# Kernel tuning notes

Hardware: AMD Instinct MI355X
Metric: run time of the kernel (lower is better)

Reference implementation:

```python
import jax, jax.numpy as jnp
import numpy as np
from jax.ops import segment_sum, segment_max

N_GENE, D_IN, HID, HEADS = 100000, 128, 128, 4
N_DRUG, N_DIS = 10000, 5000


def gcn_conv(x, src, dst, W, b, n):
    # PyG GCNConv: add self loops, symmetric deg^-1/2 normalization, scatter-add
    h = x @ W  # [n, hid]
    loop = jnp.arange(n)
    s = jnp.concatenate([src, loop])
    d = jnp.concatenate([dst, loop])
    deg = segment_sum(jnp.ones(d.shape[0], h.dtype), d, num_segments=n)
    dis = jnp.where(deg > 0, jax.lax.rsqrt(deg), 0.0)
    norm = dis[s] * dis[d]  # [E+n]
    return segment_sum(h[s] * norm[:, None], d, num_segments=n) + b


def gat_conv(xs, xd, src, dst, W, att_s, att_d, b, n_dst, heads=HEADS):
    # PyG GATConv (bipartite, shared lin, add_self_loops=False, concat=False)
    C = W.shape[1] // heads
    hs = (xs @ W).reshape(-1, heads, C)  # [Ns,H,C]
    hd = (xd @ W).reshape(-1, heads, C)  # [Nd,H,C]
    a_s = (hs * att_s).sum(-1)  # [Ns,H]
    a_d = (hd * att_d).sum(-1)  # [Nd,H]
    e = jax.nn.leaky_relu(a_s[src] + a_d[dst], 0.2)  # [E,H]
    m = segment_max(e, dst, num_segments=n_dst)
    m = jnp.where(jnp.isfinite(m), m, 0.0)
    ex = jnp.exp(e - m[dst])
    denom = segment_sum(ex, dst, num_segments=n_dst)
    alpha = ex / (denom[dst] + 1e-16)  # per-dst softmax
    out = segment_sum(hs[src] * alpha[:, :, None], dst, num_segments=n_dst)  # [Nd,H,C]
    return out.mean(axis=1) + b


def setup_inputs() -> dict:
    key = jax.random.key(0)
    ks = jax.random.split(key, 24)
    Eg, Ed, Ec = 1000000, 250000, 250000
    sc = 1.0 / np.sqrt(HID)
    inp = {
        'gene_nodes': jax.random.normal(ks[0], (N_GENE, D_IN), jnp.float32),
        'drug_edges': jnp.stack([jax.random.randint(ks[1], (Ed,), 0, N_DRUG),
                                 jax.random.randint(ks[2], (Ed,), 0, N_GENE)]),
        'disease_edges': jnp.stack([jax.random.randint(ks[3], (Ec,), 0, N_DIS),
                                    jax.random.randint(ks[4], (Ec,), 0, N_GENE)]),
        'gene_edges': jax.random.randint(ks[5], (2, Eg), 0, N_GENE),
        'gcn1_w': jax.random.normal(ks[6], (D_IN, HID), jnp.float32) * sc,
        'gcn1_b': jnp.zeros((HID,), jnp.float32),
        'gcn2_w': jax.random.normal(ks[7], (HID, HID), jnp.float32) * sc,
        'gcn2_b': jnp.zeros((HID,), jnp.float32),
        'drug_embed': jax.random.normal(ks[8], (N_DRUG, HID), jnp.float32),
        'disease_embed': jax.random.normal(ks[9], (N_DIS, HID), jnp.float32),
        'gat_d_w': jax.random.normal(ks[10], (HID, HEADS * HID), jnp.float32) * sc,
        'gat_d_att_src': jax.random.normal(ks[11], (HEADS, HID), jnp.float32) * sc,
        'gat_d_att_dst': jax.random.normal(ks[12], (HEADS, HID), jnp.float32) * sc,
        'gat_d_b': jnp.zeros((HID,), jnp.float32),
        'gat_c_w': jax.random.normal(ks[13], (HID, HEADS * HID), jnp.float32) * sc,
        'gat_c_att_src': jax.random.normal(ks[14], (HEADS, HID), jnp.float32) * sc,
        'gat_c_att_dst': jax.random.normal(ks[15], (HEADS, HID), jnp.float32) * sc,
        'gat_c_b': jnp.zeros((HID,), jnp.float32),
        'fuse_w': jax.random.normal(ks[16], (3 * HID, HID), jnp.float32) * sc,
        'fuse_b': jnp.zeros((HID,), jnp.float32),
    }
    return inp


def reference(gene_nodes, drug_edges, disease_edges, gene_edges,
              gcn1_w, gcn1_b, gcn2_w, gcn2_b, drug_embed, disease_embed,
              gat_d_w, gat_d_att_src, gat_d_att_dst, gat_d_b,
              gat_c_w, gat_c_att_src, gat_c_att_dst, gat_c_b,
              fuse_w, fuse_b):
    gs, gd = gene_edges[0], gene_edges[1]
    x = jax.nn.relu(gcn_conv(gene_nodes, gs, gd, gcn1_w, gcn1_b, N_GENE))
    x = jax.nn.relu(gcn_conv(x, gs, gd, gcn2_w, gcn2_b, N_GENE))
    # hetero GAT: drug->gene and disease->gene, HeteroConv aggr='mean'
    g_drug = gat_conv(drug_embed, x, drug_edges[0], drug_edges[1],
                      gat_d_w, gat_d_att_src, gat_d_att_dst, gat_d_b, N_GENE)
    g_dis = gat_conv(disease_embed, x, disease_edges[0], disease_edges[1],
                     gat_c_w, gat_c_att_src, gat_c_att_dst, gat_c_b, N_GENE)
    gene_out = 0.5 * (g_drug + g_dis)
    bg = gene_out.mean(axis=0, keepdims=True)   # [1,HID]
    bd = drug_embed.mean(axis=0, keepdims=True)
    bc = disease_embed.mean(axis=0, keepdims=True)
    return jnp.concatenate([bg, bd, bc], axis=-1) @ fuse_w + fuse_b  # [1,HID]
```

## Files before the change

### kernel.cpp

```cpp
#include <hip/hip_runtime.h>
#include <hip/hip_fp16.h>

#define NG 100000
#define NDR 10000
#define NDI 5000
#define NDOM (3 * NG + NDR + NDI)
#define NBUCK 616
#define BCHUNK 4096
#define EPT 16

typedef _Float16 f16x8 __attribute__((ext_vector_type(8)));
typedef float f32x4 __attribute__((ext_vector_type(4)));

__device__ __forceinline__ void atomAddF(float* p, float v) { unsafeAtomicAdd(p, v); }

static inline int cdiv_h(int a, int b) { return (a + b - 1) / b; }

__device__ __host__ __forceinline__ int bcap(int b) {
  return b < 586 ? 8192 : (b < 606 ? 24576 : 32768);
}
__device__ __host__ __forceinline__ int bbase(int b) {
  if (b < 586) return b * 8192;
  if (b < 606) return 586 * 8192 + (b - 586) * 24576;
  return 586 * 8192 + 20 * 24576 + (b - 606) * 32768;
}
#define NPAIR (586 * 8192 + 20 * 24576 + 10 * 32768)

__device__ __forceinline__ void prep_body(int blk,
                                          const float* W1, const float* W2,
                                          const float* Wd, const float* Wc,
                                          const float* attd_d, const float* attd_c,
                                          __half* Wt1, __half* Wt2,
                                          __half* Wtd, __half* Wtc, float* watt) {
  if (blk == 10) {
    int t = threadIdx.x;
    for (int slot = t; slot < 1024; slot += 256) {
      int i = slot >> 3, s8 = slot & 7;
      const float* W = (s8 < 4) ? Wd : Wc;
      const float* A = (s8 < 4) ? attd_d : attd_c;
      int h = s8 & 3;
      float s = 0.f;
      for (int cc = 0; cc < 128; cc++) s += W[(size_t)i * 512 + h * 128 + cc] * A[h * 128 + cc];
      watt[i * 8 + s8] = s;
    }
    return;
  }
  const float* W;
  __half* Wt;
  int N, base;
  if (blk == 0) { W = W1; Wt = Wt1; N = 128; base = 0; }
  else if (blk == 1) { W = W2; Wt = Wt2; N = 128; base = 0; }
  else if (blk < 6) { W = Wd; Wt = Wtd; N = 512; base = (blk - 2) * 16384; }
  else { W = Wc; Wt = Wtc; N = 512; base = (blk - 6) * 16384; }
  for (int q = threadIdx.x; q < 16384; q += 256) {
    int qq = base + q;
    int n = qq >> 7, k = qq & 127;
    Wt[qq] = __float2half(W[(size_t)k * N + n]);
  }
}

__global__ __launch_bounds__(256) void k_front(const float* __restrict__ W1,
                                               const float* __restrict__ W2,
                                               const float* __restrict__ Wd,
                                               const float* __restrict__ Wc,
                                               const float* __restrict__ attd_d,
                                               const float* __restrict__ attd_c,
                                               __half* __restrict__ Wt1,
                                               __half* __restrict__ Wt2,
                                               __half* __restrict__ Wtd,
                                               __half* __restrict__ Wtc,
                                               float* __restrict__ watt,
                                               int* __restrict__ cursor616) {
  if (blockIdx.x == 11) {
    for (int i = threadIdx.x; i < NBUCK; i += 256) cursor616[i] = bbase(i);
    return;
  }
  prep_body(blockIdx.x, W1, W2, Wd, Wc, attd_d, attd_c, Wt1, Wt2, Wtd, Wtc, watt);
}

__device__ __forceinline__ void decode(int idx, const int* __restrict__ ge, int Eg_,
                                       const int* __restrict__ de, int Ed_,
                                       const int* __restrict__ ce, int Ec_,
                                       unsigned& node, unsigned& val) {
  int B1 = Eg_, B2 = Eg_ + Ed_, B3 = Eg_ + 2 * Ed_, B4 = B3 + Ec_;
  if (idx < B1) { node = (unsigned)ge[Eg_ + idx]; val = (unsigned)ge[idx]; }
  else if (idx < B2) { int i = idx - B1; node = NG + (unsigned)de[Ed_ + i]; val = (unsigned)de[i]; }
  else if (idx < B3) { int i = idx - B2; node = 3 * NG + (unsigned)de[i]; val = (unsigned)de[Ed_ + i]; }
  else if (idx < B4) { int i = idx - B3; node = 2 * NG + (unsigned)ce[Ec_ + i]; val = (unsigned)ce[i]; }
  else { int i = idx - B4; node = 3 * NG + NDR + (unsigned)ce[i]; val = (unsigned)ce[Ec_ + i]; }
}

__global__ __launch_bounds__(256) void k_binH(const int* __restrict__ ge, int Eg_,
                                              const int* __restrict__ de, int Ed_,
                                              const int* __restrict__ ce, int Ec_,
                                              int* __restrict__ cursor616,
                                              unsigned* __restrict__ pairs) {
  __shared__ int hist[NBUCK];
  int t = threadIdx.x;
  for (int i = t; i < NBUCK; i += 256) hist[i] = 0;
  __syncthreads();
  const int ME = Eg_ + 2 * (Ed_ + Ec_);
  int base = blockIdx.x * BCHUNK;
  int cnt = min(BCHUNK, ME - base);

  unsigned nodeR[EPT], valR[EPT];
#pragma unroll
  for (int k = 0; k < EPT; k++) {
    int j = t + k * 256;
    nodeR[k] = 0xFFFFFFFFu;
    if (j < cnt) decode(base + j, ge, Eg_, de, Ed_, ce, Ec_, nodeR[k], valR[k]);
  }
#pragma unroll
  for (int k = 0; k < EPT; k++)
    if (nodeR[k] != 0xFFFFFFFFu) atomicAdd(&hist[nodeR[k] >> 9], 1);
  __syncthreads();
  for (int b = t; b < NBUCK; b += 256) {
    int h = hist[b];
    hist[b] = h ? atomicAdd(&cursor616[b], h) : 0;
  }
  __syncthreads();
#pragma unroll
  for (int k = 0; k < EPT; k++) {
    if (nodeR[k] == 0xFFFFFFFFu) continue;
    unsigned b = nodeR[k] >> 9;
    int p = atomicAdd(&hist[b], 1);
    if (p < bbase(b) + bcap(b))
      pairs[p] = ((nodeR[k] - (b << 9)) << 17) | valR[k];
  }
}

__global__ __launch_bounds__(256) void k_bucketdeg(const int* __restrict__ cursor616,
                                                   const unsigned* __restrict__ pairs,
                                                   unsigned* __restrict__ deg) {
  __shared__ int hist[512];
  int b = blockIdx.x;
  int n0 = b << 9;
  int n1 = min(n0 + 512, NDOM);
  int t = threadIdx.x;
  for (int i = t; i < 512; i += 256) hist[i] = 0;
  __syncthreads();
  int base = bbase(b);
  int cnt = min(cursor616[b] - base, bcap(b));
  for (int i = base + t; i < base + cnt; i += 256) atomicAdd(&hist[pairs[i] >> 17], 1);
  __syncthreads();
  for (int i = t; i < n1 - n0; i += 256) deg[n0 + i] = (unsigned)hist[i];
}

__global__ __launch_bounds__(256) void k_blocksum4(const unsigned* __restrict__ deg,
                                                   unsigned* __restrict__ partial, int n) {
  __shared__ unsigned s[256];
  int t = threadIdx.x;
  int base = blockIdx.x * 1024 + t * 4;
  unsigned v = 0;
  if (base + 3 < n) {
    uint4 u = *(const uint4*)&deg[base];
    v = u.x + u.y + u.z + u.w;
  } else {
    for (int j = 0; j < 4; j++)
      if (base + j < n) v += deg[base + j];
  }
  s[t] = v;
  __syncthreads();
  for (int off = 128; off; off >>= 1) {
    if (t < off) s[t] += s[t + off];
    __syncthreads();
  }
  if (!t) partial[blockIdx.x] = s[0];
}

__global__ __launch_bounds__(512) void k_scanpart(unsigned* __restrict__ partial, int nb) {
  __shared__ unsigned s[512];
  int t = threadIdx.x;
  unsigned v = (t < nb) ? partial[t] : 0u;
  s[t] = v;
  __syncthreads();
  for (int off = 1; off < 512; off <<= 1) {
    unsigned add = (t >= off) ? s[t - off] : 0u;
    __syncthreads();
    s[t] += add;
    __syncthreads();
  }
  if (t < nb) partial[t] = s[t] - v;
}

__global__ __launch_bounds__(256) void k_rowptrAll(const unsigned* __restrict__ deg,
                                                   const unsigned* __restrict__ partial, int n,
                                                   int* __restrict__ rowptr,
                                                   float* __restrict__ dis) {
  __shared__ unsigned s[256];
  int t = threadIdx.x;
  int base = blockIdx.x * 1024 + t * 4;
  unsigned v[4] = {0u, 0u, 0u, 0u};
  if (base + 3 < n) {
    uint4 u = *(const uint4*)&deg[base];
    v[0] = u.x; v[1] = u.y; v[2] = u.z; v[3] = u.w;
  } else {
    for (int j = 0; j < 4; j++)
      if (base + j < n) v[j] = deg[base + j];
  }
  unsigned sum4 = v[0] + v[1] + v[2] + v[3];
  s[t] = sum4;
  __syncthreads();
  for (int off = 1; off < 256; off <<= 1) {
    unsigned add = (t >= off) ? s[t - off] : 0u;
    __syncthreads();
    s[t] += add;
    __syncthreads();
  }
  unsigned e = s[t] - sum4 + partial[blockIdx.x];
  for (int j = 0; j < 4; j++) {
    int i = base + j;
    if (i < n) {
      rowptr[i] = (int)e;
      if (i < NG) dis[i] = rsqrtf((float)v[j] + 1.0f);
      if (i == n - 1) rowptr[n] = (int)(e + v[j]);
      e += v[j];
    }
  }
}

__global__ __launch_bounds__(256) void k_place(const int* __restrict__ rowptr,
                                               const int* __restrict__ cursor616,
                                               const unsigned* __restrict__ pairs,
                                               int* __restrict__ adj) {
  __shared__ int cur[512];
  int b = blockIdx.x;
  int n0 = b << 9;
  int n1 = min(n0 + 512, NDOM);
  int t = threadIdx.x;
  for (int i = t; i < n1 - n0; i += 256) cur[i] = rowptr[n0 + i];
  __syncthreads();
  int base = bbase(b);
  int cnt = min(cursor616[b] - base, bcap(b));
  for (int i = base + t; i < base + cnt; i += 256) {
    unsigned pr = pairs[i];
    int p = atomicAdd(&cur[pr >> 17], 1);
    adj[p] = (int)(pr & 0x1FFFFu);
  }
}

template <int INF16>
__global__ __launch_bounds__(256) void k_mgemm(const void* __restrict__ Xv,
                                               const __half* __restrict__ Wt, int M,
                                               const float* __restrict__ dis,
                                               __half* __restrict__ hh) {
  __shared__ __align__(16) char lds[48 * 1024];
  char* As = lds;
  char* Bs = lds + 16 * 1024;
  const int t = threadIdx.x;
  const int row0 = blockIdx.x * 64;

#pragma unroll
  for (int rep = 0; rep < 8; rep++) {
    int q = t + rep * 256;
    int r = q >> 4, c16 = (q & 15) * 16;
    uint4 v = *(const uint4*)((const char*)Wt + r * 256 + c16);
    *(uint4*)(Bs + ((r * 256 + c16) ^ ((r & 7) << 4))) = v;
  }
  if (INF16 == 0) {
    const float* X = (const float*)Xv;
#pragma unroll
    for (int rep = 0; rep < 8; rep++) {
      int q = t + rep * 256;
      int r = q >> 5, c4 = (q & 31) * 4;
      int gr = row0 + r;
      float4 xv = make_float4(0.f, 0.f, 0.f, 0.f);
      if (gr < M) xv = *(const float4*)&X[(size_t)gr * 128 + c4];
      __half2 h0 = __floats2half2_rn(xv.x, xv.y);
      __half2 h1 = __floats2half2_rn(xv.z, xv.w);
      uint2 pk;
      pk.x = *(unsigned*)&h0;
      pk.y = *(unsigned*)&h1;
      *(uint2*)(As + ((r * 256 + c4 * 2) ^ ((r & 7) << 4))) = pk;
    }
  } else {
    const __half* X = (const __half*)Xv;
#pragma unroll
    for (int rep = 0; rep < 4; rep++) {
      int q = t + rep * 256;
      int r = q >> 4, c16 = (q & 15) * 16;
      int gr = row0 + r;
      uint4 v = make_uint4(0u, 0u, 0u, 0u);
      if (gr < M) v = *(const uint4*)((const char*)X + (size_t)gr * 256 + c16);
      *(uint4*)(As + ((r * 256 + c16) ^ ((r & 7) << 4))) = v;
    }
  }
  __syncthreads();

  const int w = t >> 6, l = t & 63;
  const int lr = l & 15, lk = l >> 4;
  f32x4 acc[8] = {};
#pragma unroll
  for (int s = 0; s < 4; s++) {
    int arow = w * 16 + lr;
    f16x8 a = *(const f16x8*)(As + ((arow * 256 + lk * 16 + s * 64) ^ ((arow & 7) << 4)));
#pragma unroll
    for (int nt = 0; nt < 8; nt++) {
      int brow = nt * 16 + lr;
      f16x8 b = *(const f16x8*)(Bs + ((brow * 256 + lk * 16 + s * 64) ^ ((brow & 7) << 4)));
      acc[nt] = __builtin_amdgcn_mfma_f32_16x16x32_f16(a, b, acc[nt], 0, 0, 0);
    }
  }
  float ddv[4];
  int rowb = row0 + w * 16 + lk * 4;
#pragma unroll
  for (int j = 0; j < 4; j++) ddv[j] = (rowb + j < M) ? dis[rowb + j] : 0.f;
#pragma unroll
  for (int nt = 0; nt < 8; nt++) {
#pragma unroll
    for (int j = 0; j < 4; j++) {
      int row = rowb + j;
      if (row < M) hh[(size_t)row * 128 + nt * 16 + lr] = __float2half(acc[nt][j] * ddv[j]);
    }
  }
}

__global__ __launch_bounds__(256) void k_mgat(const float* __restrict__ Xd,
                                              const float* __restrict__ Xc,
                                              const __half* __restrict__ Wtd,
                                              const __half* __restrict__ Wtc,
                                              const float* __restrict__ attSd,
                                              const float* __restrict__ attSc,
                                              __half* __restrict__ hsd,
                                              __half* __restrict__ hsc,
                                              float* __restrict__ a_s_d,
                                              float* __restrict__ a_s_c) {
  __shared__ __align__(16) char lds[48 * 1024];
  char* As = lds;
  char* Bs = lds + 16 * 1024;
  const int t = threadIdx.x;
  const int nbd = (NDR + 63) >> 6;
  const int q = blockIdx.x >= nbd;
  const int bx = q ? blockIdx.x - nbd : blockIdx.x;
  const int M = q ? NDI : NDR;
  const float* X = q ? Xc : Xd;
  const __half* Wt = q ? Wtc : Wtd;
  const float* attS = q ? attSc : attSd;
  __half* hs = q ? hsc : hsd;
  float* a_s = q ? a_s_c : a_s_d;
  const int row0 = bx * 64;
  const int h = blockIdx.y;
  const __half* Wth = Wt + (size_t)h * 128 * 128;

#pragma unroll
  for (int rep = 0; rep < 8; rep++) {
    int r = (t + rep * 256) >> 4, c16 = ((t + rep * 256) & 15) * 16;
    uint4 v = *(const uint4*)((const char*)Wth + r * 256 + c16);
    *(uint4*)(Bs + ((r * 256 + c16) ^ ((r & 7) << 4))) = v;
  }
#pragma unroll
  for (int rep = 0; rep < 8; rep++) {
    int qq = t + rep * 256;
    int r = qq >> 5, c4 = (qq & 31) * 4;
    int gr = row0 + r;
    float4 xv = make_float4(0.f, 0.f, 0.f, 0.f);
    if (gr < M) xv = *(const float4*)&X[(size_t)gr * 128 + c4];
    __half2 h0 = __floats2half2_rn(xv.x, xv.y);
    __half2 h1 = __floats2half2_rn(xv.z, xv.w);
    uint2 pk;
    pk.x = *(unsigned*)&h0;
    pk.y = *(unsigned*)&h1;
    *(uint2*)(As + ((r * 256 + c4 * 2) ^ ((r & 7) << 4))) = pk;
  }
  __syncthreads();

  const int w = t >> 6, l = t & 63;
  const int lr = l & 15, lk = l >> 4;
  f32x4 acc[8] = {};
#pragma unroll
  for (int s = 0; s < 4; s++) {
    int arow = w * 16 + lr;
    f16x8 a = *(const f16x8*)(As + ((arow * 256 + lk * 16 + s * 64) ^ ((arow & 7) << 4)));
#pragma unroll
    for (int nt = 0; nt < 8; nt++) {
      int brow = nt * 16 + lr;
      f16x8 b = *(const f16x8*)(Bs + ((brow * 256 + lk * 16 + s * 64) ^ ((brow & 7) << 4)));
      acc[nt] = __builtin_amdgcn_mfma_f32_16x16x32_f16(a, b, acc[nt], 0, 0, 0);
    }
  }
  float av[8];
#pragma unroll
  for (int nt = 0; nt < 8; nt++) av[nt] = attS[h * 128 + nt * 16 + lr];

  int rowb = row0 + w * 16 + lk * 4;
  float p[4] = {0.f, 0.f, 0.f, 0.f};
#pragma unroll
  for (int nt = 0; nt < 8; nt++) {
#pragma unroll
    for (int j = 0; j < 4; j++) {
      int row = rowb + j;
      if (row < M) hs[(size_t)row * 512 + h * 128 + nt * 16 + lr] = __float2half(acc[nt][j]);
      p[j] += acc[nt][j] * av[nt];
    }
  }
#pragma unroll
  for (int m = 1; m < 16; m <<= 1) {
#pragma unroll
    for (int j = 0; j < 4; j++) p[j] += __shfl_xor(p[j], m);
  }
  if (lr == 0) {
#pragma unroll
    for (int j = 0; j < 4; j++) {
      int row = rowb + j;
      if (row < M) a_s[(size_t)row * 4 + h] = p[j];
    }
  }
}

template <int FIN>
__global__ __launch_bounds__(256) void k_gather(const __half* __restrict__ hh,
                                                const int* __restrict__ rowptr,
                                                const int* __restrict__ adj,
                                                const float* __restrict__ dis,
                                                const float* __restrict__ b,
                                                const float* __restrict__ watt,
                                                void* __restrict__ outv, int n) {
  int wid = threadIdx.x >> 6;
  int lane = threadIdx.x & 63;
  int d = blockIdx.x * 4 + wid;
  if (d >= n) return;
  int p0 = rowptr[d], p1 = rowptr[d + 1];
  int c = lane * 2;
  float2 s;
  {
    unsigned v = *(const unsigned*)&hh[(size_t)d * 128 + c];
    s = __half22float2(*(__half2*)&v);
  }
  for (int base = p0; base < p1; base += 64) {
    int remain = p1 - base;
    int m = remain < 64 ? remain : 64;
    int idx = (lane < m) ? adj[base + lane] : 0;
    int j = 0;
    for (; j + 8 <= m; j += 8) {
      int nb[8];
      unsigned v[8];
#pragma unroll
      for (int u = 0; u < 8; u++) nb[u] = __shfl(idx, j + u);
#pragma unroll
      for (int u = 0; u < 8; u++) v[u] = *(const unsigned*)&hh[(size_t)nb[u] * 128 + c];
#pragma unroll
      for (int u = 0; u < 8; u++) {
        float2 f = __half22float2(*(__half2*)&v[u]);
        s.x += f.x;
        s.y += f.y;
      }
    }
    for (; j + 4 <= m; j += 4) {
      int nb[4];
      unsigned v[4];
#pragma unroll
      for (int u = 0; u < 4; u++) nb[u] = __shfl(idx, j + u);
#pragma unroll
      for (int u = 0; u < 4; u++) v[u] = *(const unsigned*)&hh[(size_t)nb[u] * 128 + c];
#pragma unroll
      for (int u = 0; u < 4; u++) {
        float2 f = __half22float2(*(__half2*)&v[u]);
        s.x += f.x;
        s.y += f.y;
      }
    }
    for (; j < m; j++) {
      int nb = __shfl(idx, j);
      unsigned v = *(const unsigned*)&hh[(size_t)nb * 128 + c];
      float2 f = __half22float2(*(__half2*)&v);
      s.x += f.x;
      s.y += f.y;
    }
  }
  float dd = dis[d];
  float x0 = fmaxf(dd * s.x + b[c], 0.f);
  float x1v = fmaxf(dd * s.y + b[c + 1], 0.f);
  if (FIN == 1) {
    __half* o = (__half*)outv;
    __half2 hv = __floats2half2_rn(x0, x1v);
    *(__half2*)&o[(size_t)d * 128 + c] = hv;
  } else {
    float* o = (float*)outv;
    float p[8];
    const float* w0 = &watt[c * 8];
#pragma unroll
    for (int h = 0; h < 8; h++) p[h] = x0 * w0[h] + x1v * w0[8 + h];
#pragma unroll
    for (int mm = 32; mm; mm >>= 1) {
#pragma unroll
      for (int h = 0; h < 8; h++) p[h] += __shfl_xor(p[h], mm);
    }
    if (lane == 0) {
      *(float4*)&o[(size_t)d * 8] = make_float4(p[0], p[1], p[2], p[3]);
      *(float4*)&o[(size_t)d * 8 + 4] = make_float4(p[4], p[5], p[6], p[7]);
    }
  }
}

__global__ __launch_bounds__(256) void k_edgeA(const int* __restrict__ rowptr,
                                               const int* __restrict__ adj,
                                               const float* __restrict__ a_s_d,
                                               const float* __restrict__ a_s_c,
                                               const float* __restrict__ att,
                                               float* __restrict__ denom_d,
                                               float* __restrict__ denom_c) {
  int nb1 = (NG + 255) >> 8;
  int blk = blockIdx.x;
  int q = blk >= nb1;
  int d = (blk - (q ? nb1 : 0)) * 256 + threadIdx.x;
  if (d >= NG) return;
  const int* rp = rowptr + NG + (q ? NG : 0);
  const float* a_s = q ? a_s_c : a_s_d;
  float* den = q ? denom_c : denom_d;
  int p0 = rp[d], p1 = rp[d + 1];
  float4 ad4 = *(const float4*)&att[(size_t)d * 8 + q * 4];
  float4 acc = make_float4(0.f, 0.f, 0.f, 0.f);
  for (int p = p0; p < p1; p++) {
    int s = adj[p];
    float4 as4 = *(const float4*)&a_s[(size_t)s * 4];
    float v0 = as4.x + ad4.x, v1 = as4.y + ad4.y, v2 = as4.z + ad4.z, v3 = as4.w + ad4.w;
    v0 = v0 > 0.f ? v0 : 0.2f * v0;
    v1 = v1 > 0.f ? v1 : 0.2f * v1;
    v2 = v2 > 0.f ? v2 : 0.2f * v2;
    v3 = v3 > 0.f ? v3 : 0.2f * v3;
    acc.x += __expf(fminf(v0, 50.f));
    acc.y += __expf(fminf(v1, 50.f));
    acc.z += __expf(fminf(v2, 50.f));
    acc.w += __expf(fminf(v3, 50.f));
  }
  *(float4*)&den[(size_t)d * 4] = acc;
}

__global__ __launch_bounds__(256) void k_edgeB(const int* __restrict__ rowptr,
                                               const int* __restrict__ adj,
                                               const float* __restrict__ a_s_d,
                                               const float* __restrict__ a_s_c,
                                               const float* __restrict__ att,
                                               const float* __restrict__ denom_d,
                                               const float* __restrict__ denom_c,
                                               float* __restrict__ wsrc_d,
                                               float* __restrict__ wsrc_c) {
  int gw = (blockIdx.x * 256 + threadIdx.x) >> 6;
  int lane = threadIdx.x & 63;
  int q = gw >= NDR;
  int s = q ? gw - NDR : gw;
  if (q && s >= NDI) return;
  const int* rp = rowptr + 3 * NG + (q ? NDR : 0);
  const float* a_s = q ? a_s_c : a_s_d;
  const float* den = q ? denom_c : denom_d;
  float* ws = q ? wsrc_c : wsrc_d;
  int p0 = rp[s], p1 = rp[s + 1];
  float4 as4 = *(const float4*)&a_s[(size_t)s * 4];
  int attoff = q * 4;
  float4 acc = make_float4(0.f, 0.f, 0.f, 0.f);
  for (int p = p0 + lane; p < p1; p += 64) {
    int d = adj[p];
    float4 ad4 = *(const float4*)&att[(size_t)d * 8 + attoff];
    float4 dn = *(const float4*)&den[(size_t)d * 4];
    float v0 = as4.x + ad4.x, v1 = as4.y + ad4.y, v2 = as4.z + ad4.z, v3 = as4.w + ad4.w;
    v0 = v0 > 0.f ? v0 : 0.2f * v0;
    v1 = v1 > 0.f ? v1 : 0.2f * v1;
    v2 = v2 > 0.f ? v2 : 0.2f * v2;
    v3 = v3 > 0.f ? v3 : 0.2f * v3;
    acc.x += __expf(fminf(v0, 50.f)) / (dn.x + 1e-16f);
    acc.y += __expf(fminf(v1, 50.f)) / (dn.y + 1e-16f);
    acc.z += __expf(fminf(v2, 50.f)) / (dn.z + 1e-16f);
    acc.w += __expf(fminf(v3, 50.f)) / (dn.w + 1e-16f);
  }
#pragma unroll
  for (int m = 1; m < 64; m <<= 1) {
    acc.x += __shfl_xor(acc.x, m);
    acc.y += __shfl_xor(acc.y, m);
    acc.z += __shfl_xor(acc.z, m);
    acc.w += __shfl_xor(acc.w, m);
  }
  if (lane == 0) *(float4*)&ws[(size_t)s * 4] = acc;
}

__global__ __launch_bounds__(512) void k_sum(const __half* __restrict__ hs_d,
                                             const float* __restrict__ wsrc_d,
                                             float* __restrict__ S_d,
                                             const __half* __restrict__ hs_c,
                                             const float* __restrict__ wsrc_c,
                                             float* __restrict__ S_c,
                                             const float* __restrict__ xd,
                                             float* __restrict__ od,
                                             const float* __restrict__ xc,
                                             float* __restrict__ oc) {
  int t = threadIdx.x;
  const int nws_d = (NDR + 63) >> 6;
  const int nws_c = (NDI + 63) >> 6;
  const int ncs_d = (NDR + 511) >> 9;
  int blk = blockIdx.x;
  if (blk < nws_d + nws_c) {
    int q = blk >= nws_d;
    const __half* hs = q ? hs_c : hs_d;
    const float* wsrc = q ? wsrc_c : wsrc_d;
    float* S = q ? S_c : S_d;
    int N = q ? NDI : NDR;
    int r0 = (q ? blk - nws_d : blk) * 64;
    int h = t >> 7;
    int r1 = min(r0 + 64, N);
    float acc = 0.f;
    for (int r = r0; r < r1; r++) acc += wsrc[r * 4 + h] * __half2float(hs[(size_t)r * 512 + t]);
    atomAddF(&S[t], acc);
  } else {
    int cb = blk - nws_d - nws_c;
    int q = cb >= ncs_d;
    const float* x = q ? xc : xd;
    float* o = q ? oc : od;
    int N = q ? NDI : NDR;
    int r0 = (q ? cb - ncs_d : cb) * 512 + (t >> 7) * 128;
    int col = t & 127;
    int r1 = min(r0 + 128, N);
    float acc = 0.f;
    for (int r = r0; r < r1; r++) acc += x[(size_t)r * 128 + col];
    if (r0 < N) atomAddF(&o[col], acc);
  }
}

__global__ __launch_bounds__(128) void k_final(const float* __restrict__ S_d,
                                               const float* __restrict__ S_c,
                                               const float* __restrict__ bdsum,
                                               const float* __restrict__ bcsum,
                                               const float* __restrict__ bd_bias,
                                               const float* __restrict__ bc_bias,
                                               const float* __restrict__ fuse_w,
                                               const float* __restrict__ fuse_b,
                                               float* __restrict__ out) {
  __shared__ float cat[384];
  int t = threadIdx.x;
  float sd = S_d[t] + S_d[128 + t] + S_d[256 + t] + S_d[384 + t];
  float sc = S_c[t] + S_c[128 + t] + S_c[256 + t] + S_c[384 + t];
  const float inv = 1.0f / (4.0f * (float)NG);
  cat[t] = 0.5f * (sd * inv + bd_bias[t] + sc * inv + bc_bias[t]);
  cat[128 + t] = bdsum[t] * (1.0f / (float)NDR);
  cat[256 + t] = bcsum[t] * (1.0f / (float)NDI);
  __syncthreads();
  float o = fuse_b[t];
  for (int k = 0; k < 384; k++) o += cat[k] * fuse_w[k * 128 + t];
  out[t] = o;
}

extern "C" void kernel_launch(void* const* d_in, const int* in_sizes, int n_in,
                              void* d_out, int out_size, void* d_ws, size_t ws_size,
                              hipStream_t stream) {
  const float* gene_nodes   = (const float*)d_in[0];
  const int*   drug_edges   = (const int*)d_in[1];
  const int*   dise_edges   = (const int*)d_in[2];
  const int*   gene_edges   = (const int*)d_in[3];
  const float* gcn1_w       = (const float*)d_in[4];
  const float* gcn1_b       = (const float*)d_in[5];
  const float* gcn2_w       = (const float*)d_in[6];
  const float* gcn2_b       = (const float*)d_in[7];
  const float* drug_embed   = (const float*)d_in[8];
  const float* dise_embed   = (const float*)d_in[9];
  const float* gat_d_w      = (const float*)d_in[10];
  const float* gat_d_att_s  = (const float*)d_in[11];
  const float* gat_d_att_d  = (const float*)d_in[12];
  const float* gat_d_b      = (const float*)d_in[13];
  const float* gat_c_w      = (const float*)d_in[14];
  const float* gat_c_att_s  = (const float*)d_in[15];
  const float* gat_c_att_d  = (const float*)d_in[16];
  const float* gat_c_b      = (const float*)d_in[17];
  const float* fuse_w       = (const float*)d_in[18];
  const float* fuse_b       = (const float*)d_in[19];
  const int Ed = in_sizes[1] / 2;
  const int Ec = in_sizes[2] / 2;
  const int Eg = in_sizes[3] / 2;
  float* out = (float*)d_out;
  (void)n_in; (void)out_size; (void)ws_size;

  const int NBS = cdiv_h(NDOM, 1024);
  const int ME = Eg + 2 * (Ed + Ec);

  char* w = (char*)d_ws;
  auto alloc = [&](size_t n) {
    char* p = w;
    w += (n + 511) & ~(size_t)511;
    return p;
  };
  char* z0 = w;
  float* S_d        = (float*)alloc(512 * 4);
  float* S_c        = (float*)alloc(512 * 4);
  float* bdsum      = (float*)alloc(512);
  float* bcsum      = (float*)alloc(512);
  size_t zbytes = (size_t)(w - z0);
  unsigned* deg     = (unsigned*)alloc((size_t)NDOM * 4);
  float* denom_d    = (float*)alloc((size_t)NG * 16);
  float* denom_c    = (float*)alloc((size_t)NG * 16);
  float* wsrc_d     = (float*)alloc((size_t)NDR * 16);
  float* wsrc_c     = (float*)alloc((size_t)NDI * 16);
  float* dis        = (float*)alloc((size_t)NG * 4);
  float* watt       = (float*)alloc(128 * 8 * 4);
  float* att        = (float*)alloc((size_t)NG * 8 * 4);
  float* a_s_d      = (float*)alloc((size_t)NDR * 16);
  float* a_s_c      = (float*)alloc((size_t)NDI * 16);
  unsigned* partial = (unsigned*)alloc((size_t)512 * 4);
  int* rowptr       = (int*)alloc((size_t)(NDOM + 1) * 4);
  int* cursor616    = (int*)alloc((size_t)NBUCK * 4);
  int* adj          = (int*)alloc((size_t)ME * 4);
  unsigned* pairs   = (unsigned*)alloc((size_t)NPAIR * 4);
  __half* Wt1       = (__half*)alloc((size_t)128 * 128 * 2);
  __half* Wt2       = (__half*)alloc((size_t)128 * 128 * 2);
  __half* Wtd       = (__half*)alloc((size_t)512 * 128 * 2);
  __half* Wtc       = (__half*)alloc((size_t)512 * 128 * 2);
  __half* hh        = (__half*)alloc((size_t)NG * 128 * 2);
  __half* x1        = (__half*)alloc((size_t)NG * 128 * 2);
  __half* hs_d      = (__half*)alloc((size_t)NDR * 512 * 2);
  __half* hs_c      = (__half*)alloc((size_t)NDI * 512 * 2);

  hipMemsetAsync(z0, 0, zbytes, stream);

  k_front<<<12, 256, 0, stream>>>(gcn1_w, gcn2_w, gat_d_w, gat_c_w, gat_d_att_d, gat_c_att_d,
                                  Wt1, Wt2, Wtd, Wtc, watt, cursor616);

  k_binH<<<cdiv_h(ME, BCHUNK), 256, 0, stream>>>(gene_edges, Eg, drug_edges, Ed, dise_edges, Ec,
                                                 cursor616, pairs);
  k_bucketdeg<<<NBUCK, 256, 0, stream>>>(cursor616, pairs, deg);
  k_blocksum4<<<NBS, 256, 0, stream>>>(deg, partial, NDOM);
  k_scanpart<<<1, 512, 0, stream>>>(partial, NBS);
  k_rowptrAll<<<NBS, 256, 0, stream>>>(deg, partial, NDOM, rowptr, dis);
  k_place<<<NBUCK, 256, 0, stream>>>(rowptr, cursor616, pairs, adj);

  k_mgemm<0><<<cdiv_h(NG, 64), 256, 0, stream>>>(gene_nodes, Wt1, NG, dis, hh);
  k_gather<1><<<cdiv_h(NG, 4), 256, 0, stream>>>(hh, rowptr, adj, dis, gcn1_b, nullptr, x1, NG);

  k_mgemm<1><<<cdiv_h(NG, 64), 256, 0, stream>>>(x1, Wt2, NG, dis, hh);
  k_gather<2><<<cdiv_h(NG, 4), 256, 0, stream>>>(hh, rowptr, adj, dis, gcn2_b, watt, att, NG);

  k_mgat<<<dim3(cdiv_h(NDR, 64) + cdiv_h(NDI, 64), 4), 256, 0, stream>>>(
      drug_embed, dise_embed, Wtd, Wtc, gat_d_att_s, gat_c_att_s, hs_d, hs_c, a_s_d, a_s_c);

  k_edgeA<<<2 * cdiv_h(NG, 256), 256, 0, stream>>>(rowptr, adj, a_s_d, a_s_c, att, denom_d, denom_c);
  k_edgeB<<<cdiv_h((NDR + NDI) * 64, 256), 256, 0, stream>>>(rowptr, adj, a_s_d, a_s_c, att,
                                                             denom_d, denom_c, wsrc_d, wsrc_c);

  int nsum = (cdiv_h(NDR, 64) + cdiv_h(NDI, 64)) + (cdiv_h(NDR, 512) + cdiv_h(NDI, 512));
  k_sum<<<nsum, 512, 0, stream>>>(hs_d, wsrc_d, S_d, hs_c, wsrc_c, S_c,
                                  drug_embed, bdsum, dise_embed, bcsum);

  k_final<<<1, 128, 0, stream>>>(S_d, S_c, bdsum, bcsum, gat_d_b, gat_c_b, fuse_w, fuse_b, out);
}
```

Before: 369.3 us.

## Fuse CSR build into per-bucket scan and gather two nodes per wavefront

Replaces the degree/blocksum/scanpart/rowptr/place kernel chain with one small scan over bucket counts plus a single per-bucket kernel. That kernel computes the local histogram, rowptr, dis and adjacency placement from LDS, removing several launches and the global deg round trip. The GCN gather kernel now handles two destination nodes per wavefront, interleaving their neighbor loads to raise memory-level parallelism. Nodes with fewer than 64 neighbors pad the shorter list with dummy loads, which adds some wasted bandwidth, and nodes with more use a slower scalar fallback loop.

Result: faster. 361.4 us (-2.1%).

```diff
diff --git a/kernel.cpp b/kernel.cpp
--- a/kernel.cpp
+++ b/kernel.cpp
@@ -129,112 +129,85 @@
   }
 }
 
-__global__ __launch_bounds__(256) void k_bucketdeg(const int* __restrict__ cursor616,
-                                                   const unsigned* __restrict__ pairs,
-                                                   unsigned* __restrict__ deg) {
+__global__ __launch_bounds__(256) void k_scan616(const int* __restrict__ cursor616,
+                                                 int* __restrict__ bucketbase) {
+  __shared__ int s[256];
+  int t = threadIdx.x;
+  int loc[3];
+  int sum = 0;
+#pragma unroll
+  for (int k = 0; k < 3; k++) {
+    int b = 3 * t + k;
+    int v = (b < NBUCK) ? min(cursor616[b] - bbase(b), bcap(b)) : 0;
+    loc[k] = sum;
+    sum += v;
+  }
+  s[t] = sum;
+  __syncthreads();
+  for (int off = 1; off < 256; off <<= 1) {
+    int add = (t >= off) ? s[t - off] : 0;
+    __syncthreads();
+    s[t] += add;
+    __syncthreads();
+  }
+  int excl = s[t] - sum;
+#pragma unroll
+  for (int k = 0; k < 3; k++) {
+    int b = 3 * t + k;
+    if (b < NBUCK) bucketbase[b] = excl + loc[k];
+  }
+}
+
+__global__ __launch_bounds__(256) void k_placeAll(const int* __restrict__ cursor616,
+                                                  const int* __restrict__ bucketbase,
+                                                  const unsigned* __restrict__ pairs,
+                                                  int* __restrict__ rowptr,
+                                                  float* __restrict__ dis,
+                                                  int* __restrict__ adj) {
   __shared__ int hist[512];
+  __shared__ int scan[256];
   int b = blockIdx.x;
   int n0 = b << 9;
   int n1 = min(n0 + 512, NDOM);
   int t = threadIdx.x;
-  for (int i = t; i < 512; i += 256) hist[i] = 0;
+  hist[t] = 0;
+  hist[t + 256] = 0;
   __syncthreads();
   int base = bbase(b);
   int cnt = min(cursor616[b] - base, bcap(b));
   for (int i = base + t; i < base + cnt; i += 256) atomicAdd(&hist[pairs[i] >> 17], 1);
   __syncthreads();
-  for (int i = t; i < n1 - n0; i += 256) deg[n0 + i] = (unsigned)hist[i];
-}
-
-__global__ __launch_bounds__(256) void k_blocksum4(const unsigned* __restrict__ deg,
-                                                   unsigned* __restrict__ partial, int n) {
-  __shared__ unsigned s[256];
-  int t = threadIdx.x;
-  int base = blockIdx.x * 1024 + t * 4;
-  unsigned v = 0;
-  if (base + 3 < n) {
-    uint4 u = *(const uint4*)&deg[base];
-    v = u.x + u.y + u.z + u.w;
-  } else {
-    for (int j = 0; j < 4; j++)
-      if (base + j < n) v += deg[base + j];
-  }
-  s[t] = v;
-  __syncthreads();
-  for (int off = 128; off; off >>= 1) {
-    if (t < off) s[t] += s[t + off];
+  int h0 = hist[2 * t], h1 = hist[2 * t + 1];
+  int sum = h0 + h1;
+  scan[t] = sum;
+  __syncthreads();
+  for (int off = 1; off < 256; off <<= 1) {
+    int add = (t >= off) ? scan[t - off] : 0;
     __syncthreads();
-  }
-  if (!t) partial[blockIdx.x] = s[0];
-}
-
-__global__ __launch_bounds__(512) void k_scanpart(unsigned* __restrict__ partial, int nb) {
-  __shared__ unsigned s[512];
-  int t = threadIdx.x;
-  unsigned v = (t < nb) ? partial[t] : 0u;
-  s[t] = v;
-  __syncthreads();
-  for (int off = 1; off < 512; off <<= 1) {
-    unsigned add = (t >= off) ? s[t - off] : 0u;
+    scan[t] += add;
     __syncthreads();
-    s[t] += add;
-    __syncthreads();
-  }
-  if (t < nb) partial[t] = s[t] - v;
-}
-
-__global__ __launch_bounds__(256) void k_rowptrAll(const unsigned* __restrict__ deg,
-                                                   const unsigned* __restrict__ partial, int n,
-                                                   int* __restrict__ rowptr,
-                                                   float* __restrict__ dis) {
-  __shared__ unsigned s[256];
-  int t = threadIdx.x;
-  int base = blockIdx.x * 1024 + t * 4;
-  unsigned v[4] = {0u, 0u, 0u, 0u};
-  if (base + 3 < n) {
-    uint4 u = *(const uint4*)&deg[base];
-    v[0] = u.x; v[1] = u.y; v[2] = u.z; v[3] = u.w;
-  } else {
-    for (int j = 0; j < 4; j++)
-      if (base + j < n) v[j] = deg[base + j];
-  }
-  unsigned sum4 = v[0] + v[1] + v[2] + v[3];
-  s[t] = sum4;
-  __syncthreads();
-  for (int off = 1; off < 256; off <<= 1) {
-    unsigned add = (t >= off) ? s[t - off] : 0u;
-    __syncthreads();
-    s[t] += add;
-    __syncthreads();
-  }
-  unsigned e = s[t] - sum4 + partial[blockIdx.x];
-  for (int j = 0; j < 4; j++) {
-    int i = base + j;
-    if (i < n) {
-      rowptr[i] = (int)e;
-      if (i < NG) dis[i] = rsqrtf((float)v[j] + 1.0f);
-      if (i == n - 1) rowptr[n] = (int)(e + v[j]);
-      e += v[j];
-    }
-  }
-}
-
-__global__ __launch_bounds__(256) void k_place(const int* __restrict__ rowptr,
-                                               const int* __restrict__ cursor616,
-                                               const unsigned* __restrict__ pairs,
-                                               int* __restrict__ adj) {
-  __shared__ int cur[512];
-  int b = blockIdx.x;
-  int n0 = b << 9;
-  int n1 = min(n0 + 512, NDOM);
-  int t = threadIdx.x;
-  for (int i = t; i < n1 - n0; i += 256) cur[i] = rowptr[n0 + i];
-  __syncthreads();
-  int base = bbase(b);
-  int cnt = min(cursor616[b] - base, bcap(b));
+  }
+  int excl = scan[t] - sum;
+  int bb = bucketbase[b];
+  int i0 = 2 * t, i1 = 2 * t + 1;
+  int r0 = bb + excl, r1 = bb + excl + h0;
+  if (n0 + i0 < n1) {
+    rowptr[n0 + i0] = r0;
+    if (n0 + i0 < NG) dis[n0 + i0] = rsqrtf((float)h0 + 1.0f);
+  }
+  if (n0 + i1 < n1) {
+    rowptr[n0 + i1] = r1;
+    if (n0 + i1 < NG) dis[n0 + i1] = rsqrtf((float)h1 + 1.0f);
+    if (n0 + i1 == NDOM - 1) rowptr[NDOM] = r1 + h1;
+  }
+  if (n0 + i0 == NDOM - 1) rowptr[NDOM] = r0 + h0;
+  __syncthreads();
+  hist[i0] = r0;
+  hist[i1] = r1;
+  __syncthreads();
   for (int i = base + t; i < base + cnt; i += 256) {
     unsigned pr = pairs[i];
-    int p = atomicAdd(&cur[pr >> 17], 1);
+    int p = atomicAdd(&hist[pr >> 17], 1);
     adj[p] = (int)(pr & 0x1FFFFu);
   }
 }
@@ -417,77 +390,117 @@
                                                 void* __restrict__ outv, int n) {
   int wid = threadIdx.x >> 6;
   int lane = threadIdx.x & 63;
-  int d = blockIdx.x * 4 + wid;
-  if (d >= n) return;
-  int p0 = rowptr[d], p1 = rowptr[d + 1];
+  int d0 = blockIdx.x * 8 + wid * 2;
+  if (d0 >= n) return;
+  int d1 = d0 + 1;
+  bool hasB = (d1 < n);
+  int p0a = rowptr[d0], p1a = rowptr[d0 + 1];
+  int p0b = p1a, p1b = hasB ? rowptr[d1 + 1] : p1a;
   int c = lane * 2;
-  float2 s;
+  float2 sA, sB = make_float2(0.f, 0.f);
   {
-    unsigned v = *(const unsigned*)&hh[(size_t)d * 128 + c];
-    s = __half22float2(*(__half2*)&v);
-  }
-  for (int base = p0; base < p1; base += 64) {
-    int remain = p1 - base;
-    int m = remain < 64 ? remain : 64;
-    int idx = (lane < m) ? adj[base + lane] : 0;
-    int j = 0;
-    for (; j + 8 <= m; j += 8) {
+    unsigned v = *(const unsigned*)&hh[(size_t)d0 * 128 + c];
+    sA = __half22float2(*(__half2*)&v);
+  }
+  if (hasB) {
+    unsigned v = *(const unsigned*)&hh[(size_t)d1 * 128 + c];
+    sB = __half22float2(*(__half2*)&v);
+  }
+  int mA = p1a - p0a, mB = p1b - p0b;
+  if (mA <= 64 && mB <= 64) {
+    int idxA = (lane < mA) ? adj[p0a + lane] : 0;
+    int idxB = (lane < mB) ? adj[p0b + lane] : 0;
+    int M = mA > mB ? mA : mB;
+    for (int j = 0; j < M; j += 4) {
       int nb[8];
+      bool ok[8];
+#pragma unroll
+      for (int u = 0; u < 4; u++) {
+        int ja = j + u;
+        int va = __shfl(idxA, ja & 63);
+        ok[u] = ja < mA;
+        nb[u] = ok[u] ? va : d0;
+        int vb = __shfl(idxB, ja & 63);
+        ok[4 + u] = ja < mB;
+        nb[4 + u] = ok[4 + u] ? vb : d0;
+      }
       unsigned v[8];
 #pragma unroll
-      for (int u = 0; u < 8; u++) nb[u] = __shfl(idx, j + u);
-#pragma unroll
       for (int u = 0; u < 8; u++) v[u] = *(const unsigned*)&hh[(size_t)nb[u] * 128 + c];
-#pragma unroll
-      for (int u = 0; u < 8; u++) {
-        float2 f = __half22float2(*(__half2*)&v[u]);
-        s.x += f.x;
-        s.y += f.y;
-      }
-    }
-    for (; j + 4 <= m; j += 4) {
-      int nb[4];
-      unsigned v[4];
-#pragma unroll
-      for (int u = 0; u < 4; u++) nb[u] = __shfl(idx, j + u);
-#pragma unroll
-      for (int u = 0; u < 4; u++) v[u] = *(const unsigned*)&hh[(size_t)nb[u] * 128 + c];
 #pragma unroll
       for (int u = 0; u < 4; u++) {
         float2 f = __half22float2(*(__half2*)&v[u]);
-        s.x += f.x;
-        s.y += f.y;
+        if (ok[u]) { sA.x += f.x; sA.y += f.y; }
       }
-    }
-    for (; j < m; j++) {
-      int nb = __shfl(idx, j);
-      unsigned v = *(const unsigned*)&hh[(size_t)nb * 128 + c];
-      float2 f = __half22float2(*(__half2*)&v);
-      s.x += f.x;
-      s.y += f.y;
-    }
-  }
-  float dd = dis[d];
-  float x0 = fmaxf(dd * s.x + b[c], 0.f);
-  float x1v = fmaxf(dd * s.y + b[c + 1], 0.f);
+#pragma unroll
+      for (int u = 4; u < 8; u++) {
+        float2 f = __half22float2(*(__half2*)&v[u]);
+        if (ok[u]) { sB.x += f.x; sB.y += f.y; }
+      }
+    }
+  } else {
+    for (int base = p0a; base < p1a; base += 64) {
+      int m = min(p1a - base, 64);
+      int idx = (lane < m) ? adj[base + lane] : 0;
+      for (int j = 0; j < m; j++) {
+        int nb = __shfl(idx, j);
+        unsigned v = *(const unsigned*)&hh[(size_t)nb * 128 + c];
+        float2 f = __half22float2(*(__half2*)&v);
+        sA.x += f.x;
+        sA.y += f.y;
+      }
+    }
+    for (int base = p0b; base < p1b; base += 64) {
+      int m = min(p1b - base, 64);
+      int idx = (lane < m) ? adj[base + lane] : 0;
+      for (int j = 0; j < m; j++) {
+        int nb = __shfl(idx, j);
+        unsigned v = *(const unsigned*)&hh[(size_t)nb * 128 + c];
+        float2 f = __half22float2(*(__half2*)&v);
+        sB.x += f.x;
+        sB.y += f.y;
+      }
+    }
+  }
+  float ddA = dis[d0];
+  float ddB = hasB ? dis[d1] : 0.f;
+  float bc0 = b[c], bc1 = b[c + 1];
+  float xA0 = fmaxf(ddA * sA.x + bc0, 0.f);
+  float xA1 = fmaxf(ddA * sA.y + bc1, 0.f);
+  float xB0 = fmaxf(ddB * sB.x + bc0, 0.f);
+  float xB1 = fmaxf(ddB * sB.y + bc1, 0.f);
   if (FIN == 1) {
     __half* o = (__half*)outv;
-    __half2 hv = __floats2half2_rn(x0, x1v);
-    *(__half2*)&o[(size_t)d * 128 + c] = hv;
+    __half2 hA = __floats2half2_rn(xA0, xA1);
+    *(__half2*)&o[(size_t)d0 * 128 + c] = hA;
+    if (hasB) {
+      __half2 hB = __floats2half2_rn(xB0, xB1);
+      *(__half2*)&o[(size_t)d1 * 128 + c] = hB;
+    }
   } else {
     float* o = (float*)outv;
-    float p[8];
+    float pA[8], pB[8];
     const float* w0 = &watt[c * 8];
 #pragma unroll
-    for (int h = 0; h < 8; h++) p[h] = x0 * w0[h] + x1v * w0[8 + h];
+    for (int h = 0; h < 8; h++) {
+      pA[h] = xA0 * w0[h] + xA1 * w0[8 + h];
+      pB[h] = xB0 * w0[h] + xB1 * w0[8 + h];
+    }
 #pragma unroll
     for (int mm = 32; mm; mm >>= 1) {
 #pragma unroll
-      for (int h = 0; h < 8; h++) p[h] += __shfl_xor(p[h], mm);
+      for (int h = 0; h < 8; h++) {
+        pA[h] += __shfl_xor(pA[h], mm);
+        pB[h] += __shfl_xor(pB[h], mm);
+      }
     }
     if (lane == 0) {
-      *(float4*)&o[(size_t)d * 8] = make_float4(p[0], p[1], p[2], p[3]);
-      *(float4*)&o[(size_t)d * 8 + 4] = make_float4(p[4], p[5], p[6], p[7]);
+      *(float4*)&o[(size_t)d0 * 8] = make_float4(pA[0], pA[1], pA[2], pA[3]);
+      *(float4*)&o[(size_t)d0 * 8 + 4] = make_float4(pA[4], pA[5], pA[6], pA[7]);
+      if (hasB) {
+        *(float4*)&o[(size_t)d1 * 8] = make_float4(pB[0], pB[1], pB[2], pB[3]);
+        *(float4*)&o[(size_t)d1 * 8 + 4] = make_float4(pB[4], pB[5], pB[6], pB[7]);
+      }
     }
   }
 }
@@ -666,7 +679,6 @@
   float* out = (float*)d_out;
   (void)n_in; (void)out_size; (void)ws_size;
 
-  const int NBS = cdiv_h(NDOM, 1024);
   const int ME = Eg + 2 * (Ed + Ec);
 
   char* w = (char*)d_ws;
@@ -681,7 +693,6 @@
   float* bdsum      = (float*)alloc(512);
   float* bcsum      = (float*)alloc(512);
   size_t zbytes = (size_t)(w - z0);
-  unsigned* deg     = (unsigned*)alloc((size_t)NDOM * 4);
   float* denom_d    = (float*)alloc((size_t)NG * 16);
   float* denom_c    = (float*)alloc((size_t)NG * 16);
   float* wsrc_d     = (float*)alloc((size_t)NDR * 16);
@@ -691,9 +702,9 @@
   float* att        = (float*)alloc((size_t)NG * 8 * 4);
   float* a_s_d      = (float*)alloc((size_t)NDR * 16);
   float* a_s_c      = (float*)alloc((size_t)NDI * 16);
-  unsigned* partial = (unsigned*)alloc((size_t)512 * 4);
   int* rowptr       = (int*)alloc((size_t)(NDOM + 1) * 4);
   int* cursor616    = (int*)alloc((size_t)NBUCK * 4);
+  int* bucketbase   = (int*)alloc((size_t)(NBUCK + 1) * 4);
   int* adj          = (int*)alloc((size_t)ME * 4);
   unsigned* pairs   = (unsigned*)alloc((size_t)NPAIR * 4);
   __half* Wt1       = (__half*)alloc((size_t)128 * 128 * 2);
@@ -712,17 +723,14 @@
 
   k_binH<<<cdiv_h(ME, BCHUNK), 256, 0, stream>>>(gene_edges, Eg, drug_edges, Ed, dise_edges, Ec,
                                                  cursor616, pairs);
-  k_bucketdeg<<<NBUCK, 256, 0, stream>>>(cursor616, pairs, deg);
-  k_blocksum4<<<NBS, 256, 0, stream>>>(deg, partial, NDOM);
-  k_scanpart<<<1, 512, 0, stream>>>(partial, NBS);
-  k_rowptrAll<<<NBS, 256, 0, stream>>>(deg, partial, NDOM, rowptr, dis);
-  k_place<<<NBUCK, 256, 0, stream>>>(rowptr, cursor616, pairs, adj);
+  k_scan616<<<1, 256, 0, stream>>>(cursor616, bucketbase);
+  k_placeAll<<<NBUCK, 256, 0, stream>>>(cursor616, bucketbase, pairs, rowptr, dis, adj);
 
   k_mgemm<0><<<cdiv_h(NG, 64), 256, 0, stream>>>(gene_nodes, Wt1, NG, dis, hh);
-  k_gather<1><<<cdiv_h(NG, 4), 256, 0, stream>>>(hh, rowptr, adj, dis, gcn1_b, nullptr, x1, NG);
+  k_gather<1><<<cdiv_h(NG, 8), 256, 0, stream>>>(hh, rowptr, adj, dis, gcn1_b, nullptr, x1, NG);
 
   k_mgemm<1><<<cdiv_h(NG, 64), 256, 0, stream>>>(x1, Wt2, NG, dis, hh);
-  k_gather<2><<<cdiv_h(NG, 4), 256, 0, stream>>>(hh, rowptr, adj, dis, gcn2_b, watt, att, NG);
+  k_gather<2><<<cdiv_h(NG, 8), 256, 0, stream>>>(hh, rowptr, adj, dis, gcn2_b, watt, att, NG);
 
   k_mgat<<<dim3(cdiv_h(NDR, 64) + cdiv_h(NDI, 64), 4), 256, 0, stream>>>(
       drug_embed, dise_embed, Wtd, Wtc, gat_d_att_s, gat_c_att_s, hs_d, hs_c, a_s_d, a_s_c);
```
